# Optimization experiments

Hardware: AMD Instinct MI355X
Metric: run time of the kernel (lower is better)

## Reference

```python
import jax, jax.numpy as jnp
import numpy as np

B, S, DIM = 2, 2048, 2048
QH, KVH = 32, 8
HD = DIM // QH            # 64
KV_DIM = HD * KVH         # 512
MAX_LEN = 2048
SCALE = HD ** -0.5
NEG_INF = -1e30


def _rope_cache(seq_len, head_dim, max_len, theta=10000.0, factor=8.0):
    # faithful to generate_sin_cos_pos_emb (causal branch, offset=0),
    # cache built at max_len then sliced to seq_len by the caller
    idx = np.arange(0, head_dim, 2, dtype=np.float64) / head_dim
    inv_freq = 1.0 / theta ** idx
    if factor > 1.0:
        seq_eff = max(max_len, max_len)  # generate called with seq_len=max_length
        adj = (factor * seq_eff / max_len - (factor - 1.0)) ** (head_dim / (head_dim - 2.0))
        inv_freq = 1.0 / (theta * adj) ** idx
    pos = np.arange(0, max_len, dtype=np.float64)
    freqs = np.einsum('i,j->ij', pos, inv_freq)
    emb = np.concatenate([freqs, freqs], axis=-1)  # [max_len, head_dim]
    cos = jnp.asarray(np.cos(emb)[:seq_len], dtype=jnp.float32)
    sin = jnp.asarray(np.sin(emb)[:seq_len], dtype=jnp.float32)
    return cos, sin


def _rotate_half(x):
    x1, x2 = jnp.split(x, 2, axis=-1)
    return jnp.concatenate([-x2, x1], axis=-1)


def _apply_rope(x, cos, sin):
    # x: [B, H, S, D]; cos/sin: [S, D]
    return x * cos + _rotate_half(x) * sin


def setup_inputs() -> dict:
    key = jax.random.key(0)
    ks = jax.random.split(key, 11)
    s = 0.02
    return {
        'query': jax.random.normal(ks[0], (B, S, DIM), jnp.float32),
        'key':   jax.random.normal(ks[1], (B, S, DIM), jnp.float32),
        'value': jax.random.normal(ks[2], (B, S, DIM), jnp.float32),
        'w_q': jax.random.normal(ks[3], (DIM, DIM), jnp.float32) * s,
        'b_q': jnp.zeros((DIM,), jnp.float32),
        'w_k': jax.random.normal(ks[4], (DIM, KV_DIM), jnp.float32) * s,
        'b_k': jnp.zeros((KV_DIM,), jnp.float32),
        'w_v': jax.random.normal(ks[5], (DIM, KV_DIM), jnp.float32) * s,
        'b_v': jnp.zeros((KV_DIM,), jnp.float32),
        'w_o': jax.random.normal(ks[6], (DIM, DIM), jnp.float32) * s,
        'b_o': jnp.zeros((DIM,), jnp.float32),
    }


def reference(query, key, value, w_q, b_q, w_k, b_k, w_v, b_v, w_o, b_o):
    # projections (weights stored as [in, out])
    q = query @ w_q + b_q                                    # [B,S,DIM]
    k = key   @ w_k + b_k                                    # [B,S,KV_DIM]
    v = value @ w_v + b_v                                    # [B,S,KV_DIM]

    q = q.reshape(B, S, QH, HD).transpose(0, 2, 1, 3)        # [B,QH,S,HD]
    k = k.reshape(B, S, KVH, HD).transpose(0, 2, 1, 3)       # [B,KVH,S,HD]
    v = v.reshape(B, S, KVH, HD).transpose(0, 2, 1, 3)       # [B,KVH,S,HD]

    cos, sin = _rope_cache(S, HD, MAX_LEN)
    q = _apply_rope(q, cos, sin)
    k = _apply_rope(k, cos, sin)

    # GQA: group queries per kv head (equivalent to repeat_interleave on K/V)
    G = QH // KVH
    qg = q.reshape(B, KVH, G, S, HD)
    scores = jnp.einsum('bhgqd,bhkd->bhgqk', qg, k) * SCALE  # [B,KVH,G,S,S]
    causal = jnp.tril(jnp.ones((S, S), dtype=bool))
    scores = jnp.where(causal, scores, NEG_INF)
    probs = jax.nn.softmax(scores, axis=-1)
    ctx = jnp.einsum('bhgqk,bhkd->bhgqd', probs, v)          # [B,KVH,G,S,HD]
    ctx = ctx.reshape(B, QH, S, HD).transpose(0, 2, 1, 3).reshape(B, S, DIM)
    return ctx @ w_o + b_o                                   # [B,S,DIM]
```

## Files before the change

kernel.cpp:

```cpp
#include <hip/hip_runtime.h>
#include <hip/hip_bf16.h>

typedef __hip_bfloat16 bf16_t;
typedef __attribute__((ext_vector_type(8))) short bf16x8;
typedef __attribute__((ext_vector_type(4))) float f32x4;
typedef __attribute__((ext_vector_type(16))) float f32x16;

#define S_LEN   2048
#define D_MODEL 2048
#define N_QH    32
#define N_KVH   8
#define HEAD_D  64
#define KV_D    512
#define M_ROWS  4096
#define QK_SCALE (0.125f * 1.44269504088896340736f)
#define NQT     16

struct __align__(8) bf16x4s { bf16_t x, y, z, w; };

__global__ void prep_kernel(const float* __restrict__ wq, const float* __restrict__ wk,
                            const float* __restrict__ wv, const float* __restrict__ wo,
                            bf16_t* __restrict__ tq, bf16_t* __restrict__ tk,
                            bf16_t* __restrict__ tv, bf16_t* __restrict__ to,
                            const float* __restrict__ query, const float* __restrict__ key_,
                            const float* __restrict__ value,
                            bf16_t* __restrict__ qbf, bf16_t* __restrict__ kbf,
                            bf16_t* __restrict__ vbf,
                            float* __restrict__ cosT, float* __restrict__ sinT) {
    const int bx = blockIdx.x, t = threadIdx.x;
    if (bx < 10240) {
        __shared__ float tile[32][33];
        const float* W; bf16_t* Wt; int N, nb, kt;
        if (bx < 4096)      { W = wq; Wt = tq; N = D_MODEL; nb = bx & 63;          kt = bx >> 6; }
        else if (bx < 5120) { int i = bx - 4096; W = wk; Wt = tk; N = KV_D; nb = i & 15; kt = i >> 4; }
        else if (bx < 6144) { int i = bx - 5120; W = wv; Wt = tv; N = KV_D; nb = i & 15; kt = i >> 4; }
        else                { int i = bx - 6144; W = wo; Wt = to; N = D_MODEL; nb = i & 63; kt = i >> 6; }
        const int K = D_MODEL;
        int n0 = nb * 32, k0 = kt * 32;
        int tx = t & 31, ty = t >> 5;
#pragma unroll
        for (int i = 0; i < 4; i++) {
            int r = ty + i * 8;
            tile[r][tx] = W[(size_t)(k0 + r) * N + n0 + tx];
        }
        __syncthreads();
#pragma unroll
        for (int i = 0; i < 4; i++) {
            int r = ty + i * 8;
            Wt[(size_t)(n0 + r) * K + k0 + tx] = __float2bfloat16(tile[tx][r]);
        }
        return;
    }
    if (bx < 10304) {
        int blk = bx - 10240;
        int j = t & 31;
        double invf = pow(10000.0, -(double)(2 * j) / 64.0);
#pragma unroll
        for (int i = 0; i < 4; i++) {
            int pos = blk * 32 + i * 8 + (t >> 5);
            double a = (double)pos * invf;
            cosT[pos * 32 + j] = (float)cos(a);
            sinT[pos * 32 + j] = (float)sin(a);
        }
        return;
    }
    const int per = M_ROWS * D_MODEL / 4;
    int tid = (bx - 10304) * 256 + t;
    for (int i = tid; i < 3 * per; i += 1536 * 256) {
        const float* src; bf16_t* dst; int off;
        if (i < per)          { src = query; dst = qbf; off = i; }
        else if (i < 2 * per) { src = key_;  dst = kbf; off = i - per; }
        else                  { src = value; dst = vbf; off = i - 2 * per; }
        float4 v = ((const float4*)src)[off];
        bf16x4s o;
        o.x = __float2bfloat16(v.x);
        o.y = __float2bfloat16(v.y);
        o.z = __float2bfloat16(v.z);
        o.w = __float2bfloat16(v.w);
        ((bf16x4s*)dst)[off] = o;
    }
}

__device__ __forceinline__ void async_copy16(const bf16_t* g, bf16_t* l) {
    __builtin_amdgcn_global_load_lds((const __attribute__((address_space(1))) void*)g,
                                     (__attribute__((address_space(3))) void*)l, 16, 0, 0);
}

template <int ROPE, int OUTF32, int QSCALE>
__global__ __launch_bounds__(256, 2)
void gqa_gemm_kernel(const bf16_t* __restrict__ A, const bf16_t* __restrict__ Bt,
                     const float* __restrict__ bias, void* __restrict__ Cout,
                     int M, int N, int K,
                     const float* __restrict__ cosT, const float* __restrict__ sinT) {
    __shared__ __align__(16) bf16_t As[128 * 64];
    __shared__ __align__(16) bf16_t Bs[128 * 64];

    const int t = threadIdx.x;
    const int bx = blockIdx.x;
    const int xcd = bx & 7, j = bx >> 3;
    const int am0 = (((xcd >> 1) << 3) + (j >> 3)) * 128;
    const int bn0 = (((xcd & 1) << 3) + (j & 7)) * 128;

    const int l = t & 63, w = t >> 6;
    const int wr = w >> 1, wc = w & 1;
    const int lr = l & 15, lk = l >> 4;

    f32x4 acc[4][4];
#pragma unroll
    for (int i = 0; i < 4; i++)
#pragma unroll
        for (int jx = 0; jx < 4; jx++) acc[i][jx] = (f32x4)0.0f;

    const int r0 = t >> 3;
    const int c  = (t & 7) ^ (r0 & 7);
    const bf16_t* aptr = A + (size_t)(am0 + r0) * K + c * 8;
    const bf16_t* bptr = Bt + (size_t)(bn0 + r0) * K + c * 8;
    bf16_t* aLds = As + r0 * 64 + (t & 7) * 8;
    bf16_t* bLds = Bs + r0 * 64 + (t & 7) * 8;

    for (int k0 = 0; k0 < K; k0 += 64) {
#pragma unroll
        for (int s = 0; s < 4; ++s) {
            async_copy16(aptr + (size_t)(s * 32) * K + k0, aLds + s * 2048);
            async_copy16(bptr + (size_t)(s * 32) * K + k0, bLds + s * 2048);
        }
        __syncthreads();

        bf16x8 af[4][2], bfr[4][2];
#pragma unroll
        for (int mi = 0; mi < 4; mi++)
#pragma unroll
            for (int ks = 0; ks < 2; ks++)
                af[mi][ks] = *(const bf16x8*)&As[(wr * 64 + mi * 16 + lr) * 64 +
                                 ((ks * 32 + lk * 8) ^ ((lr & 7) << 3))];
#pragma unroll
        for (int ni = 0; ni < 4; ni++)
#pragma unroll
            for (int ks = 0; ks < 2; ks++)
                bfr[ni][ks] = *(const bf16x8*)&Bs[(wc * 64 + ni * 16 + lr) * 64 +
                                  ((ks * 32 + lk * 8) ^ ((lr & 7) << 3))];
#pragma unroll
        for (int mi = 0; mi < 4; mi++)
#pragma unroll
            for (int ni = 0; ni < 4; ni++)
#pragma unroll
                for (int ks = 0; ks < 2; ks++)
                    acc[mi][ni] = __builtin_amdgcn_mfma_f32_16x16x32_bf16(
                        af[mi][ks], bfr[ni][ks], acc[mi][ni], 0, 0, 0);
        __syncthreads();
    }

#pragma unroll
    for (int mi = 0; mi < 4; mi++) {
#pragma unroll
        for (int reg = 0; reg < 4; reg++) {
            int row = am0 + wr * 64 + mi * 16 + lk * 4 + reg;
            if (OUTF32) {
                float* out = (float*)Cout;
#pragma unroll
                for (int ni = 0; ni < 4; ni++) {
                    int col = bn0 + wc * 64 + ni * 16 + lr;
                    out[(size_t)row * N + col] = acc[mi][ni][reg] + bias[col];
                }
            } else if (ROPE) {
                bf16_t* out = (bf16_t*)Cout;
                int pos = row & (S_LEN - 1);
#pragma unroll
                for (int np = 0; np < 2; np++) {
                    int jj = np * 16 + lr;
                    float cs = cosT[pos * 32 + jj];
                    float sn = sinT[pos * 32 + jj];
                    int col1 = bn0 + wc * 64 + np * 16 + lr;
                    float x1 = acc[mi][np][reg] + bias[col1];
                    float x2 = acc[mi][np + 2][reg] + bias[col1 + 32];
                    float o1 = x1 * cs - x2 * sn;
                    float o2 = x2 * cs + x1 * sn;
                    if (QSCALE) { o1 *= QK_SCALE; o2 *= QK_SCALE; }
                    out[(size_t)row * N + col1]      = __float2bfloat16(o1);
                    out[(size_t)row * N + col1 + 32] = __float2bfloat16(o2);
                }
            } else {
                bf16_t* out = (bf16_t*)Cout;
#pragma unroll
                for (int ni = 0; ni < 4; ni++) {
                    int col = bn0 + wc * 64 + ni * 16 + lr;
                    out[(size_t)row * N + col] =
                        __float2bfloat16(acc[mi][ni][reg] + bias[col]);
                }
            }
        }
    }
}

__global__ __launch_bounds__(256, 2)
void gqa_qkv_kernel(const bf16_t* __restrict__ Qbf, const bf16_t* __restrict__ Kbf,
                    const bf16_t* __restrict__ Vbf,
                    const bf16_t* __restrict__ Wtq, const bf16_t* __restrict__ Wtk,
                    const bf16_t* __restrict__ Wtv,
                    const float* __restrict__ bq, const float* __restrict__ bk,
                    const float* __restrict__ bv,
                    bf16_t* __restrict__ Qout, bf16_t* __restrict__ Kout,
                    bf16_t* __restrict__ VtOut,
                    const float* __restrict__ cosT, const float* __restrict__ sinT) {
    __shared__ __align__(16) char smem[128 * 140 * 2];
    bf16_t* As = (bf16_t*)smem;
    bf16_t* Bs = (bf16_t*)(smem + 16384);
    bf16_t* TT = (bf16_t*)smem;

    const int t = threadIdx.x, bx = blockIdx.x;
    constexpr int K = D_MODEL;

    int am0, bn0, mode;
    const bf16_t *A, *Bt; const float* bias;
    if (bx < 512) {
        int xcd = bx & 7, j = bx >> 3;
        am0 = (((xcd >> 1) << 3) + (j >> 3)) * 128;
        bn0 = (((xcd & 1) << 3) + (j & 7)) * 128;
        A = Qbf; Bt = Wtq; bias = bq; mode = 0;
    } else {
        int idx = bx - 512;
        int z = idx >> 7;
        int xcd = idx & 7, jj = (idx & 127) >> 3;
        am0 = (xcd * 4 + (jj & 3)) * 128;
        bn0 = (jj >> 2) * 128;
        A = z ? Vbf : Kbf; Bt = z ? Wtv : Wtk; bias = z ? bv : bk; mode = z ? 2 : 1;
    }

    const int l = t & 63, w = t >> 6;
    const int wr = w >> 1, wc = w & 1;
    const int lr = l & 15, lk = l >> 4;

    f32x4 acc[4][4];
#pragma unroll
    for (int i = 0; i < 4; i++)
#pragma unroll
        for (int jx = 0; jx < 4; jx++) acc[i][jx] = (f32x4)0.0f;

    const int r0 = t >> 3;
    const int c  = (t & 7) ^ (r0 & 7);
    const bf16_t* aptr = A + (size_t)(am0 + r0) * K + c * 8;
    const bf16_t* bptr = Bt + (size_t)(bn0 + r0) * K + c * 8;
    bf16_t* aLds = As + r0 * 64 + (t & 7) * 8;
    bf16_t* bLds = Bs + r0 * 64 + (t & 7) * 8;

    for (int k0 = 0; k0 < K; k0 += 64) {
#pragma unroll
        for (int s = 0; s < 4; ++s) {
            async_copy16(aptr + (size_t)(s * 32) * K + k0, aLds + s * 2048);
            async_copy16(bptr + (size_t)(s * 32) * K + k0, bLds + s * 2048);
        }
        __syncthreads();

        bf16x8 af[4][2], bfr[4][2];
#pragma unroll
        for (int mi = 0; mi < 4; mi++)
#pragma unroll
            for (int ks = 0; ks < 2; ks++)
                af[mi][ks] = *(const bf16x8*)&As[(wr * 64 + mi * 16 + lr) * 64 +
                                 ((ks * 32 + lk * 8) ^ ((lr & 7) << 3))];
#pragma unroll
        for (int ni = 0; ni < 4; ni++)
#pragma unroll
            for (int ks = 0; ks < 2; ks++)
                bfr[ni][ks] = *(const bf16x8*)&Bs[(wc * 64 + ni * 16 + lr) * 64 +
                                  ((ks * 32 + lk * 8) ^ ((lr & 7) << 3))];
#pragma unroll
        for (int mi = 0; mi < 4; mi++)
#pragma unroll
            for (int ni = 0; ni < 4; ni++)
#pragma unroll
                for (int ks = 0; ks < 2; ks++)
                    acc[mi][ni] = __builtin_amdgcn_mfma_f32_16x16x32_bf16(
                        af[mi][ks], bfr[ni][ks], acc[mi][ni], 0, 0, 0);
        __syncthreads();
    }

    if (mode == 2) {
#pragma unroll
        for (int mi = 0; mi < 4; mi++)
#pragma unroll
            for (int ni = 0; ni < 4; ni++) {
                int colL = wc * 64 + ni * 16 + lr;
                float bz = bias[bn0 + colL];
                bf16x4s pk;
                pk.x = __float2bfloat16(acc[mi][ni][0] + bz);
                pk.y = __float2bfloat16(acc[mi][ni][1] + bz);
                pk.z = __float2bfloat16(acc[mi][ni][2] + bz);
                pk.w = __float2bfloat16(acc[mi][ni][3] + bz);
                *(bf16x4s*)&TT[colL * 140 + wr * 64 + mi * 16 + lk * 4] = pk;
            }
        __syncthreads();
        const int colL = t >> 1, s0 = (t & 1) * 64;
        const int cg = bn0 + colL;
        const int bI = am0 >> 11;
        bf16_t* dst = VtOut + ((size_t)(bI * N_KVH + (cg >> 6)) * HEAD_D + (cg & 63)) * S_LEN
                      + (am0 & (S_LEN - 1)) + s0;
        const bf16_t* src = &TT[colL * 140 + s0];
#pragma unroll
        for (int i = 0; i < 8; i++)
            *(bf16x8*)(dst + i * 8) = *(const bf16x8*)(src + i * 8);
        return;
    }

    const int N = (mode == 0) ? D_MODEL : KV_D;
    bf16_t* out = (mode == 0) ? Qout : Kout;
    const float qs = (mode == 0) ? QK_SCALE : 1.0f;
#pragma unroll
    for (int mi = 0; mi < 4; mi++)
#pragma unroll
        for (int reg = 0; reg < 4; reg++) {
            int row = am0 + wr * 64 + mi * 16 + lk * 4 + reg;
            int pos = row & (S_LEN - 1);
#pragma unroll
            for (int np = 0; np < 2; np++) {
                int jj = np * 16 + lr;
                float cs = cosT[pos * 32 + jj];
                float sn = sinT[pos * 32 + jj];
                int col1 = bn0 + wc * 64 + np * 16 + lr;
                float x1 = acc[mi][np][reg] + bias[col1];
                float x2 = acc[mi][np + 2][reg] + bias[col1 + 32];
                out[(size_t)row * N + col1]      = __float2bfloat16((x1 * cs - x2 * sn) * qs);
                out[(size_t)row * N + col1 + 32] = __float2bfloat16((x2 * cs + x1 * sn) * qs);
            }
        }
}

__device__ __forceinline__ void stage_K4(const bf16_t* KB, bf16_t* dst, int kt, int t) {
    const int skey = t >> 3;
    const int c    = (t & 7) ^ (skey & 7);
#pragma unroll
    for (int s = 0; s < 2; ++s)
        async_copy16(KB + (size_t)(kt * 64 + s * 32 + skey) * KV_D + c * 8,
                     dst + s * 2048 + t * 8);
}
__device__ __forceinline__ void stage_V4(const bf16_t* VTb, bf16_t* dst, int kt, int t) {
    const int sd = t >> 3;
    const int c  = (t & 7) ^ (sd & 7);
#pragma unroll
    for (int s = 0; s < 2; ++s)
        async_copy16(VTb + (size_t)(s * 32 + sd) * S_LEN + kt * 64 + c * 8,
                     dst + s * 2048 + t * 8);
}

__global__ __launch_bounds__(256, 3)
void gqa_attn_kernel(const bf16_t* __restrict__ Q, const bf16_t* __restrict__ Kb,
                     const bf16_t* __restrict__ VT, bf16_t* __restrict__ Ctx) {
    __shared__ __align__(16) bf16_t Ks[2][64 * 64];
    __shared__ __align__(16) bf16_t Vs[2][64 * 64];
    __shared__ __align__(16) bf16_t Pw[4][32 * 72];

    const int t = threadIdx.x, l = t & 63, w = t >> 6;
    const int lq = l & 31;
    const int hi = l >> 5;

    const int flat = blockIdx.x;
    const int xcd = flat & 7, j0 = flat >> 3;
    const int qt  = NQT - 1 - (j0 >> 3);
    const int rem = j0 & 7;
    const int combo = xcd * 2 + (rem >> 2);
    const int b   = combo >> 3;
    const int kvh = combo & 7;
    const int h   = kvh * 4 + (rem & 3);

    const bf16_t* KB  = Kb + (size_t)b * S_LEN * KV_D + kvh * HEAD_D;
    const bf16_t* VTb = VT + ((size_t)(b * N_KVH + kvh) * HEAD_D) * S_LEN;

    const int q0w = qt * 128 + w * 32;
    const int qg  = q0w + lq;

    bf16x8 qf[4];
    {
        const bf16_t* qrow = Q + ((size_t)(b * S_LEN + qg)) * D_MODEL + h * HEAD_D;
#pragma unroll
        for (int s = 0; s < 4; s++)
            qf[s] = *(const bf16x8*)(qrow + s * 16 + hi * 8);
    }

    f32x16 oaccT[2];
    oaccT[0] = (f32x16)0.0f;
    oaccT[1] = (f32x16)0.0f;
    float lrow = 0.f;

    const int nkt = 2 * qt + 2;

    stage_K4(KB, Ks[0], 0, t);
    stage_V4(VTb, Vs[0], 0, t);
    __syncthreads();

    int cur = 0;
    for (int kt = 0; kt < nkt; ++kt) {
        const bool pre = (kt + 1 < nkt);
        if (pre) {
            stage_K4(KB, Ks[cur ^ 1], kt + 1, t);
            stage_V4(VTb, Vs[cur ^ 1], kt + 1, t);
        }

        if (kt * 64 <= q0w + 31) {
            const bool diag = (kt * 64 + 63 > q0w);

            f32x16 sfr[2];
            sfr[0] = (f32x16)0.0f;
            sfr[1] = (f32x16)0.0f;
            __builtin_amdgcn_s_setprio(1);
#pragma unroll
            for (int kh = 0; kh < 2; kh++)
#pragma unroll
                for (int s = 0; s < 4; s++) {
                    bf16x8 kf = *(const bf16x8*)&Ks[cur][(kh * 32 + lq) * 64 +
                                    ((s * 16 + hi * 8) ^ ((lq & 7) << 3))];
                    sfr[kh] = __builtin_amdgcn_mfma_f32_32x32x16_bf16(kf, qf[s],
                                                                      sfr[kh], 0, 0, 0);
                }
            __builtin_amdgcn_s_setprio(0);

            float rs = 0.f;
#pragma unroll
            for (int kh = 0; kh < 2; kh++)
#pragma unroll
                for (int rq = 0; rq < 4; rq++) {
                    int keybase = kt * 64 + kh * 32 + rq * 8 + hi * 4;
                    float sc0 = sfr[kh][rq * 4 + 0];
                    float sc1 = sfr[kh][rq * 4 + 1];
                    float sc2 = sfr[kh][rq * 4 + 2];
                    float sc3 = sfr[kh][rq * 4 + 3];
                    if (diag) {
                        if (keybase + 0 > qg) sc0 = -1e30f;
                        if (keybase + 1 > qg) sc1 = -1e30f;
                        if (keybase + 2 > qg) sc2 = -1e30f;
                        if (keybase + 3 > qg) sc3 = -1e30f;
                    }
                    float e0 = exp2f(sc0), e1 = exp2f(sc1);
                    float e2 = exp2f(sc2), e3 = exp2f(sc3);
                    rs += (e0 + e1) + (e2 + e3);
                    unsigned u0 = __builtin_bit_cast(unsigned, e0);
                    unsigned u1 = __builtin_bit_cast(unsigned, e1);
                    unsigned u2 = __builtin_bit_cast(unsigned, e2);
                    unsigned u3 = __builtin_bit_cast(unsigned, e3);
                    uint2 pk;
                    pk.x = (u0 >> 16) | (u1 & 0xFFFF0000u);
                    pk.y = (u2 >> 16) | (u3 & 0xFFFF0000u);
                    *(uint2*)&Pw[w][lq * 72 + kh * 32 + rq * 8 + hi * 4] = pk;
                }
            lrow += rs;

            __builtin_amdgcn_s_setprio(1);
#pragma unroll
            for (int kk = 0; kk < 4; kk++) {
                bf16x8 pf = *(const bf16x8*)&Pw[w][lq * 72 + kk * 16 + hi * 8];
#pragma unroll
                for (int df = 0; df < 2; df++) {
                    bf16x8 vf = *(const bf16x8*)&Vs[cur][(df * 32 + lq) * 64 +
                                    ((kk * 16 + hi * 8) ^ ((lq & 7) << 3))];
                    oaccT[df] = __builtin_amdgcn_mfma_f32_32x32x16_bf16(vf, pf,
                                        oaccT[df], 0, 0, 0);
                }
            }
            __builtin_amdgcn_s_setprio(0);
        }

        __syncthreads();
        cur ^= 1;
    }

    {
        float lsum = lrow + __shfl_xor(lrow, 32);
        float inv = 1.0f / lsum;
        bf16_t* crow = Ctx + ((size_t)(b * S_LEN + qg)) * D_MODEL + h * HEAD_D;
#pragma unroll
        for (int df = 0; df < 2; df++)
#pragma unroll
            for (int rq = 0; rq < 4; rq++) {
                bf16x4s ov;
                ov.x = __float2bfloat16(oaccT[df][rq * 4 + 0] * inv);
                ov.y = __float2bfloat16(oaccT[df][rq * 4 + 1] * inv);
                ov.z = __float2bfloat16(oaccT[df][rq * 4 + 2] * inv);
                ov.w = __float2bfloat16(oaccT[df][rq * 4 + 3] * inv);
                *(bf16x4s*)(crow + df * 32 + rq * 8 + hi * 4) = ov;
            }
    }
}

extern "C" void kernel_launch(void* const* d_in, const int* in_sizes, int n_in,
                              void* d_out, int out_size, void* d_ws, size_t ws_size,
                              hipStream_t stream) {
    const float* query = (const float*)d_in[0];
    const float* key_  = (const float*)d_in[1];
    const float* value = (const float*)d_in[2];
    const float* w_q = (const float*)d_in[3];
    const float* b_q = (const float*)d_in[4];
    const float* w_k = (const float*)d_in[5];
    const float* b_k = (const float*)d_in[6];
    const float* w_v = (const float*)d_in[7];
    const float* b_v = (const float*)d_in[8];
    const float* w_o = (const float*)d_in[9];
    const float* b_o = (const float*)d_in[10];
    float* out = (float*)d_out;

    char* ws = (char*)d_ws;
    bf16_t* qbf  = (bf16_t*)(ws);
    bf16_t* qb   = (bf16_t*)(ws + (size_t)(16 << 20));
    bf16_t* kb   = (bf16_t*)(ws + (size_t)(32 << 20));
    bf16_t* vt   = (bf16_t*)(ws + (size_t)(36 << 20));
    bf16_t* wtq  = (bf16_t*)(ws + (size_t)(40 << 20));
    bf16_t* wtk  = (bf16_t*)(ws + (size_t)(48 << 20));
    bf16_t* wtv  = (bf16_t*)(ws + (size_t)(50 << 20));
    bf16_t* wto  = (bf16_t*)(ws + (size_t)(52 << 20));
    float* cosT  = (float*)(ws + (size_t)(60 << 20));
    float* sinT  = (float*)(ws + (size_t)(60 << 20) + (256 << 10));
    bf16_t* kbf  = (bf16_t*)(ws + (size_t)(61 << 20));
    bf16_t* vbf  = (bf16_t*)(ws + (size_t)(77 << 20));

    prep_kernel<<<11840, 256, 0, stream>>>(w_q, w_k, w_v, w_o, wtq, wtk, wtv, wto,
                                           query, key_, value, qbf, kbf, vbf, cosT, sinT);

    gqa_qkv_kernel<<<768, 256, 0, stream>>>(qbf, kbf, vbf, wtq, wtk, wtv,
                                            b_q, b_k, b_v, qb, kb, vt, cosT, sinT);

    gqa_attn_kernel<<<1024, 256, 0, stream>>>(qb, kb, vt, qbf);

    gqa_gemm_kernel<0, 1, 0><<<512, 256, 0, stream>>>(
        qbf, wto, b_o, out, M_ROWS, D_MODEL, D_MODEL, cosT, sinT);
}
```

Measured before the change: 202.4 us.

## Fuse fp32-to-bf16 activation conversion into QKV projection GEMM with register prefetch

```diff
diff --git a/kernel.cpp b/kernel.cpp
--- a/kernel.cpp
+++ b/kernel.cpp
@@ -22,10 +22,6 @@
                             const float* __restrict__ wv, const float* __restrict__ wo,
                             bf16_t* __restrict__ tq, bf16_t* __restrict__ tk,
                             bf16_t* __restrict__ tv, bf16_t* __restrict__ to,
-                            const float* __restrict__ query, const float* __restrict__ key_,
-                            const float* __restrict__ value,
-                            bf16_t* __restrict__ qbf, bf16_t* __restrict__ kbf,
-                            bf16_t* __restrict__ vbf,
                             float* __restrict__ cosT, float* __restrict__ sinT) {
     const int bx = blockIdx.x, t = threadIdx.x;
     if (bx < 10240) {
@@ -51,33 +47,15 @@
         }
         return;
     }
-    if (bx < 10304) {
-        int blk = bx - 10240;
-        int j = t & 31;
-        double invf = pow(10000.0, -(double)(2 * j) / 64.0);
-#pragma unroll
-        for (int i = 0; i < 4; i++) {
-            int pos = blk * 32 + i * 8 + (t >> 5);
-            double a = (double)pos * invf;
-            cosT[pos * 32 + j] = (float)cos(a);
-            sinT[pos * 32 + j] = (float)sin(a);
-        }
-        return;
-    }
-    const int per = M_ROWS * D_MODEL / 4;
-    int tid = (bx - 10304) * 256 + t;
-    for (int i = tid; i < 3 * per; i += 1536 * 256) {
-        const float* src; bf16_t* dst; int off;
-        if (i < per)          { src = query; dst = qbf; off = i; }
-        else if (i < 2 * per) { src = key_;  dst = kbf; off = i - per; }
-        else                  { src = value; dst = vbf; off = i - 2 * per; }
-        float4 v = ((const float4*)src)[off];
-        bf16x4s o;
-        o.x = __float2bfloat16(v.x);
-        o.y = __float2bfloat16(v.y);
-        o.z = __float2bfloat16(v.z);
-        o.w = __float2bfloat16(v.w);
-        ((bf16x4s*)dst)[off] = o;
+    int blk = bx - 10240;
+    int j = t & 31;
+    double invf = pow(10000.0, -(double)(2 * j) / 64.0);
+#pragma unroll
+    for (int i = 0; i < 4; i++) {
+        int pos = blk * 32 + i * 8 + (t >> 5);
+        double a = (double)pos * invf;
+        cosT[pos * 32 + j] = (float)cos(a);
+        sinT[pos * 32 + j] = (float)sin(a);
     }
 }
 
@@ -193,8 +171,8 @@
 }
 
 __global__ __launch_bounds__(256, 2)
-void gqa_qkv_kernel(const bf16_t* __restrict__ Qbf, const bf16_t* __restrict__ Kbf,
-                    const bf16_t* __restrict__ Vbf,
+void gqa_qkv_kernel(const float* __restrict__ Qf, const float* __restrict__ Kf,
+                    const float* __restrict__ Vf,
                     const bf16_t* __restrict__ Wtq, const bf16_t* __restrict__ Wtk,
                     const bf16_t* __restrict__ Wtv,
                     const float* __restrict__ bq, const float* __restrict__ bk,
@@ -209,21 +187,22 @@
 
     const int t = threadIdx.x, bx = blockIdx.x;
     constexpr int K = D_MODEL;
+    constexpr int NT = K / 64;
 
     int am0, bn0, mode;
-    const bf16_t *A, *Bt; const float* bias;
+    const float* A32; const bf16_t* Bt; const float* bias;
     if (bx < 512) {
         int xcd = bx & 7, j = bx >> 3;
         am0 = (((xcd >> 1) << 3) + (j >> 3)) * 128;
         bn0 = (((xcd & 1) << 3) + (j & 7)) * 128;
-        A = Qbf; Bt = Wtq; bias = bq; mode = 0;
+        A32 = Qf; Bt = Wtq; bias = bq; mode = 0;
     } else {
         int idx = bx - 512;
         int z = idx >> 7;
         int xcd = idx & 7, jj = (idx & 127) >> 3;
         am0 = (xcd * 4 + (jj & 3)) * 128;
         bn0 = (jj >> 2) * 128;
-        A = z ? Vbf : Kbf; Bt = z ? Wtv : Wtk; bias = z ? bv : bk; mode = z ? 2 : 1;
+        A32 = z ? Vf : Kf; Bt = z ? Wtv : Wtk; bias = z ? bv : bk; mode = z ? 2 : 1;
     }
 
     const int l = t & 63, w = t >> 6;
@@ -236,20 +215,44 @@
 #pragma unroll
         for (int jx = 0; jx < 4; jx++) acc[i][jx] = (f32x4)0.0f;
 
+    const int ar = t >> 1, ah = t & 1;
+    const float* aBase = A32 + (size_t)(am0 + ar) * K + ah * 32;
     const int r0 = t >> 3;
     const int c  = (t & 7) ^ (r0 & 7);
-    const bf16_t* aptr = A + (size_t)(am0 + r0) * K + c * 8;
     const bf16_t* bptr = Bt + (size_t)(bn0 + r0) * K + c * 8;
-    bf16_t* aLds = As + r0 * 64 + (t & 7) * 8;
     bf16_t* bLds = Bs + r0 * 64 + (t & 7) * 8;
 
-    for (int k0 = 0; k0 < K; k0 += 64) {
-#pragma unroll
-        for (int s = 0; s < 4; ++s) {
-            async_copy16(aptr + (size_t)(s * 32) * K + k0, aLds + s * 2048);
-            async_copy16(bptr + (size_t)(s * 32) * K + k0, bLds + s * 2048);
-        }
-        __syncthreads();
+    float4 pa[8];
+#pragma unroll
+    for (int q = 0; q < 8; q++) pa[q] = ((const float4*)aBase)[q];
+
+    for (int it = 0; it < NT; ++it) {
+#pragma unroll
+        for (int ci = 0; ci < 4; ci++) {
+            union { bf16x8 v; bf16_t e[8]; } u;
+            float4 a0 = pa[2 * ci], a1 = pa[2 * ci + 1];
+            u.e[0] = __float2bfloat16(a0.x); u.e[1] = __float2bfloat16(a0.y);
+            u.e[2] = __float2bfloat16(a0.z); u.e[3] = __float2bfloat16(a0.w);
+            u.e[4] = __float2bfloat16(a1.x); u.e[5] = __float2bfloat16(a1.y);
+            u.e[6] = __float2bfloat16(a1.z); u.e[7] = __float2bfloat16(a1.w);
+            *(bf16x8*)&As[ar * 64 + (((ah << 2) + ci) ^ (ar & 7)) * 8] = u.v;
+        }
+#pragma unroll
+        for (int s = 0; s < 4; ++s)
+            async_copy16(bptr + (size_t)(s * 32) * K + it * 64, bLds + s * 2048);
+        __builtin_amdgcn_sched_barrier(0);
+        if (it + 1 < NT) {
+            const float* ap = aBase + (it + 1) * 64;
+#pragma unroll
+            for (int q = 0; q < 8; q++) pa[q] = ((const float4*)ap)[q];
+            __builtin_amdgcn_sched_barrier(0);
+            asm volatile("s_waitcnt vmcnt(8) lgkmcnt(0)" ::: "memory");
+        } else {
+            asm volatile("s_waitcnt vmcnt(0) lgkmcnt(0)" ::: "memory");
+        }
+        __builtin_amdgcn_sched_barrier(0);
+        __builtin_amdgcn_s_barrier();
+        __builtin_amdgcn_sched_barrier(0);
 
         bf16x8 af[4][2], bfr[4][2];
 #pragma unroll
@@ -272,10 +275,13 @@
                 for (int ks = 0; ks < 2; ks++)
                     acc[mi][ni] = __builtin_amdgcn_mfma_f32_16x16x32_bf16(
                         af[mi][ks], bfr[ni][ks], acc[mi][ni], 0, 0, 0);
+        __builtin_amdgcn_sched_barrier(0);
+        __builtin_amdgcn_s_barrier();
+        __builtin_amdgcn_sched_barrier(0);
+    }
+
+    if (mode == 2) {
         __syncthreads();
-    }
-
-    if (mode == 2) {
 #pragma unroll
         for (int mi = 0; mi < 4; mi++)
 #pragma unroll
@@ -497,7 +503,7 @@
     float* out = (float*)d_out;
 
     char* ws = (char*)d_ws;
-    bf16_t* qbf  = (bf16_t*)(ws);
+    bf16_t* ctxb = (bf16_t*)(ws);
     bf16_t* qb   = (bf16_t*)(ws + (size_t)(16 << 20));
     bf16_t* kb   = (bf16_t*)(ws + (size_t)(32 << 20));
     bf16_t* vt   = (bf16_t*)(ws + (size_t)(36 << 20));
@@ -507,17 +513,15 @@
     bf16_t* wto  = (bf16_t*)(ws + (size_t)(52 << 20));
     float* cosT  = (float*)(ws + (size_t)(60 << 20));
     float* sinT  = (float*)(ws + (size_t)(60 << 20) + (256 << 10));
-    bf16_t* kbf  = (bf16_t*)(ws + (size_t)(61 << 20));
-    bf16_t* vbf  = (bf16_t*)(ws + (size_t)(77 << 20));
-
-    prep_kernel<<<11840, 256, 0, stream>>>(w_q, w_k, w_v, w_o, wtq, wtk, wtv, wto,
-                                           query, key_, value, qbf, kbf, vbf, cosT, sinT);
-
-    gqa_qkv_kernel<<<768, 256, 0, stream>>>(qbf, kbf, vbf, wtq, wtk, wtv,
+
+    prep_kernel<<<10304, 256, 0, stream>>>(w_q, w_k, w_v, w_o, wtq, wtk, wtv, wto,
+                                           cosT, sinT);
+
+    gqa_qkv_kernel<<<768, 256, 0, stream>>>(query, key_, value, wtq, wtk, wtv,
                                             b_q, b_k, b_v, qb, kb, vt, cosT, sinT);
 
-    gqa_attn_kernel<<<1024, 256, 0, stream>>>(qb, kb, vt, qbf);
+    gqa_attn_kernel<<<1024, 256, 0, stream>>>(qb, kb, vt, ctxb);
 
     gqa_gemm_kernel<0, 1, 0><<<512, 256, 0, stream>>>(
-        qbf, wto, b_o, out, M_ROWS, D_MODEL, D_MODEL, cosT, sinT);
-}
+        ctxb, wto, b_o, out, M_ROWS, D_MODEL, D_MODEL, cosT, sinT);
+}
```

New measurement: 241.2 us. 1.19x slower.
